# Performance work log

Measured on AMD Instinct MI355X. Metric: run time of the kernel, lower is better.

Reference implementation:

```python
import jax, jax.numpy as jnp
import numpy as np
import math

B, S, D, H, F = 2, 2048, 1024, 16, 4096
HD = D // H  # head size 64
EPS = 1e-5


def layernorm(x, g, b):
    mu = jnp.mean(x, axis=-1, keepdims=True)
    var = jnp.mean((x - mu) ** 2, axis=-1, keepdims=True)
    return (x - mu) * jax.lax.rsqrt(var + EPS) * g + b


def new_gelu(x):
    c = math.sqrt(2.0 / math.pi)
    return 0.5 * x * (1.0 + jnp.tanh(c * (x + 0.044715 * x ** 3)))


def setup_inputs() -> dict:
    key = jax.random.key(0)
    ks = jax.random.split(key, 20)
    sc = 0.02
    return {
        "x": jax.random.normal(ks[0], (B, S, D), jnp.float32),
        # per-head q/k/v weights stacked: [H, HD, D] (torch Linear weight layout [out,in])
        "Wq": jax.random.normal(ks[1], (H, HD, D), jnp.float32) * sc,
        "bq": jax.random.normal(ks[2], (H, HD), jnp.float32) * sc,
        "Wk": jax.random.normal(ks[3], (H, HD, D), jnp.float32) * sc,
        "bk": jax.random.normal(ks[4], (H, HD), jnp.float32) * sc,
        "Wv": jax.random.normal(ks[5], (H, HD, D), jnp.float32) * sc,
        "bv": jax.random.normal(ks[6], (H, HD), jnp.float32) * sc,
        "Wo": jax.random.normal(ks[7], (D, D), jnp.float32) * sc,
        "bo": jax.random.normal(ks[8], (D,), jnp.float32) * sc,
        "ln1_g": 1.0 + jax.random.normal(ks[9], (D,), jnp.float32) * sc,
        "ln1_b": jax.random.normal(ks[10], (D,), jnp.float32) * sc,
        "W1": jax.random.normal(ks[11], (F, D), jnp.float32) * sc,
        "b1": jax.random.normal(ks[12], (F,), jnp.float32) * sc,
        "W2": jax.random.normal(ks[13], (D, F), jnp.float32) * sc,
        "b2": jax.random.normal(ks[14], (D,), jnp.float32) * sc,
        "ln2_g": 1.0 + jax.random.normal(ks[15], (D,), jnp.float32) * sc,
        "ln2_b": jax.random.normal(ks[16], (D,), jnp.float32) * sc,
    }


def reference(x, Wq, bq, Wk, bk, Wv, bv, Wo, bo, ln1_g, ln1_b, W1, b1, W2, b2, ln2_g, ln2_b):
    # --- pre-LN multi-head attention (dropout is identity in eval) ---
    h = layernorm(x, ln1_g, ln1_b)
    q = jnp.einsum("bsd,hed->bshe", h, Wq) + bq  # [B,S,H,HD]
    k = jnp.einsum("bsd,hed->bshe", h, Wk) + bk
    v = jnp.einsum("bsd,hed->bshe", h, Wv) + bv
    scores = jnp.einsum("bshe,bthe->bhst", q, k) / math.sqrt(HD)
    probs = jax.nn.softmax(scores, axis=-1)
    attn = jnp.einsum("bhst,bthe->bshe", probs, v).reshape(B, S, D)  # concat heads
    attn = attn @ Wo.T + bo
    x = x + attn
    # --- pre-LN MLP with NewGELU ---
    h2 = layernorm(x, ln2_g, ln2_b)
    mlp = new_gelu(h2 @ W1.T + b1) @ W2.T + b2
    return x + mlp
```

## Files before the change

### kernel.cpp

```cpp
#include <hip/hip_runtime.h>

typedef unsigned short u16;
typedef __attribute__((ext_vector_type(8))) __bf16 bf16x8;
typedef __attribute__((ext_vector_type(4))) __bf16 bf16x4;
typedef __attribute__((ext_vector_type(4))) float f32x4;
typedef __attribute__((ext_vector_type(4))) unsigned short u16x4;

#define AS1 __attribute__((address_space(1)))
#define AS3 __attribute__((address_space(3)))

__device__ __forceinline__ void async_load16(const void* g, void* l) {
  __builtin_amdgcn_global_load_lds((const AS1 void*)g, (AS3 void*)l, 16, 0, 0);
}

__device__ __forceinline__ float exp2_fast(float x) {
#if __has_builtin(__builtin_amdgcn_exp2f)
  return __builtin_amdgcn_exp2f(x);
#else
  return exp2f(x);
#endif
}
__device__ __forceinline__ float rcp_fast(float x) {
#if __has_builtin(__builtin_amdgcn_rcpf)
  return __builtin_amdgcn_rcpf(x);
#else
  return 1.0f / x;
#endif
}

__device__ __forceinline__ u16 f2bf(float f) {
  union { float f; unsigned u; } a; a.f = f;
  unsigned u = a.u;
  u += 0x7fffu + ((u >> 16) & 1u);
  return (u16)(u >> 16);
}
__device__ __forceinline__ u16 bf_bits(float f) {
  union { __bf16 b; u16 u; } c; c.b = (__bf16)f; return c.u;
}

__global__ __launch_bounds__(256)
void f2b_kernel(const float* __restrict__ s, u16* __restrict__ d, int n4) {
  int i = blockIdx.x * 256 + threadIdx.x;
  if (i >= n4) return;
  const float4 v = ((const float4*)s)[i];
  u16x4 o; o[0] = f2bf(v.x); o[1] = f2bf(v.y); o[2] = f2bf(v.z); o[3] = f2bf(v.w);
  ((u16x4*)d)[i] = o;
}

__global__ __launch_bounds__(256)
void ln_kernel(const float* __restrict__ x, const float* __restrict__ g,
               const float* __restrict__ b, u16* __restrict__ out) {
  const int row = blockIdx.x, tid = threadIdx.x;
  const float4 v = ((const float4*)(x + (size_t)row * 1024))[tid];
  float s = v.x + v.y + v.z + v.w;
  float s2 = v.x * v.x + v.y * v.y + v.z * v.z + v.w * v.w;
#pragma unroll
  for (int o = 1; o < 64; o <<= 1) { s += __shfl_xor(s, o); s2 += __shfl_xor(s2, o); }
  __shared__ float red[8];
  const int wave = tid >> 6, lane = tid & 63;
  if (lane == 0) { red[wave] = s; red[wave + 4] = s2; }
  __syncthreads();
  s = red[0] + red[1] + red[2] + red[3];
  s2 = red[4] + red[5] + red[6] + red[7];
  const float mu = s * (1.f / 1024.f);
  const float rstd = rsqrtf(s2 * (1.f / 1024.f) - mu * mu + 1e-5f);
  const float4 gg = ((const float4*)g)[tid];
  const float4 bb = ((const float4*)b)[tid];
  u16x4 o4;
  o4[0] = f2bf((v.x - mu) * rstd * gg.x + bb.x);
  o4[1] = f2bf((v.y - mu) * rstd * gg.y + bb.y);
  o4[2] = f2bf((v.z - mu) * rstd * gg.z + bb.z);
  o4[3] = f2bf((v.w - mu) * rstd * gg.w + bb.w);
  ((u16x4*)(out + (size_t)row * 1024))[tid] = o4;
}

__global__ __launch_bounds__(256)
void ln_fuse(const float* __restrict__ x, const float* __restrict__ p0,
             const float* __restrict__ p1, const float* __restrict__ bo,
             const float* __restrict__ g, const float* __restrict__ b,
             float* __restrict__ out, u16* __restrict__ hb) {
  const int row = blockIdx.x, tid = threadIdx.x;
  const size_t base = (size_t)row * 1024;
  const float4 xv = ((const float4*)(x + base))[tid];
  const float4 a0 = ((const float4*)(p0 + base))[tid];
  const float4 a1 = ((const float4*)(p1 + base))[tid];
  const float4 bv = ((const float4*)bo)[tid];
  float4 t;
  t.x = xv.x + a0.x + a1.x + bv.x;
  t.y = xv.y + a0.y + a1.y + bv.y;
  t.z = xv.z + a0.z + a1.z + bv.z;
  t.w = xv.w + a0.w + a1.w + bv.w;
  ((float4*)(out + base))[tid] = t;
  float s = t.x + t.y + t.z + t.w;
  float s2 = t.x * t.x + t.y * t.y + t.z * t.z + t.w * t.w;
#pragma unroll
  for (int o = 1; o < 64; o <<= 1) { s += __shfl_xor(s, o); s2 += __shfl_xor(s2, o); }
  __shared__ float red[8];
  const int wave = tid >> 6, lane = tid & 63;
  if (lane == 0) { red[wave] = s; red[wave + 4] = s2; }
  __syncthreads();
  s = red[0] + red[1] + red[2] + red[3];
  s2 = red[4] + red[5] + red[6] + red[7];
  const float mu = s * (1.f / 1024.f);
  const float rstd = rsqrtf(s2 * (1.f / 1024.f) - mu * mu + 1e-5f);
  const float4 gg = ((const float4*)g)[tid];
  const float4 bb = ((const float4*)b)[tid];
  u16x4 o4;
  o4[0] = f2bf((t.x - mu) * rstd * gg.x + bb.x);
  o4[1] = f2bf((t.y - mu) * rstd * gg.y + bb.y);
  o4[2] = f2bf((t.z - mu) * rstd * gg.z + bb.z);
  o4[3] = f2bf((t.w - mu) * rstd * gg.w + bb.w);
  ((u16x4*)(hb + base))[tid] = o4;
}

__global__ __launch_bounds__(256)
void add2(float* __restrict__ out, const float* __restrict__ m0,
          const float* __restrict__ m1, const float* __restrict__ b2) {
  const int i = blockIdx.x * 256 + threadIdx.x;
  const float4 o = ((const float4*)out)[i];
  const float4 a = ((const float4*)m0)[i];
  const float4 c = ((const float4*)m1)[i];
  const float4 bv = ((const float4*)b2)[i & 255];
  float4 r;
  r.x = o.x + a.x + c.x + bv.x;
  r.y = o.y + a.y + c.y + bv.y;
  r.z = o.z + a.z + c.z + bv.z;
  r.w = o.w + a.w + c.w + bv.w;
  ((float4*)out)[i] = r;
}

template <class Epi>
__global__ __launch_bounds__(256)
void gemm_bt(const u16* __restrict__ A, const u16* __restrict__ Bw,
             int ldk, int K, Epi epi) {
  __shared__ __align__(16) u16 As[128 * 32];
  __shared__ __align__(16) u16 Bs[128 * 32];
  const int tid = threadIdx.x;
  const int wave = tid >> 6, lane = tid & 63;
  const int quad = lane >> 4, l16 = lane & 15;
  const int bm = blockIdx.x * 128, bn = blockIdx.y * 128;
  const int kz = blockIdx.z;
  const int wm = (wave & 1) * 64, wn = (wave >> 1) * 64;

  const int srow = lane >> 2, scol = (lane & 3) * 8;
  const u16* pa0 = A + (size_t)(bm + wave * 32 + srow) * ldk + (size_t)kz * K + scol;
  const u16* pa1 = pa0 + (size_t)16 * ldk;
  const u16* pb0 = Bw + (size_t)(bn + wave * 32 + srow) * ldk + (size_t)kz * K + scol;
  const u16* pb1 = pb0 + (size_t)16 * ldk;
  u16* la0 = &As[wave * 1024];
  u16* la1 = la0 + 512;
  u16* lb0 = &Bs[wave * 1024];
  u16* lb1 = lb0 + 512;

  const f32x4 fz = {0.f, 0.f, 0.f, 0.f};
  f32x4 acc[4][4];
#pragma unroll
  for (int i = 0; i < 4; i++)
#pragma unroll
    for (int j = 0; j < 4; j++) acc[i][j] = fz;

  for (int k0 = 0; k0 < K; k0 += 32) {
    async_load16(pa0, la0);
    async_load16(pa1, la1);
    async_load16(pb0, lb0);
    async_load16(pb1, lb1);
    pa0 += 32; pa1 += 32; pb0 += 32; pb1 += 32;
    __syncthreads();
    bf16x8 af[4], bfr[4];
#pragma unroll
    for (int mi = 0; mi < 4; mi++)
      af[mi] = *(const bf16x8*)&As[(wm + mi * 16 + l16) * 32 + quad * 8];
#pragma unroll
    for (int ni = 0; ni < 4; ni++)
      bfr[ni] = *(const bf16x8*)&Bs[(wn + ni * 16 + l16) * 32 + quad * 8];
#pragma unroll
    for (int mi = 0; mi < 4; mi++)
#pragma unroll
      for (int ni = 0; ni < 4; ni++)
        acc[mi][ni] = __builtin_amdgcn_mfma_f32_16x16x32_bf16(af[mi], bfr[ni], acc[mi][ni], 0, 0, 0);
    __syncthreads();
  }
#pragma unroll
  for (int mi = 0; mi < 4; mi++)
#pragma unroll
    for (int ni = 0; ni < 4; ni++)
      epi(bm + wm + mi * 16 + quad * 4, bn + wn + ni * 16 + l16, kz, acc[mi][ni]);
}

struct EpiQKV {
  u16 *q, *k, *vt; const float *bq, *bk, *bv;
  __device__ void operator()(int m0, int n, int, f32x4 v) const {
    const int which = n >> 10, nn = n & 1023;
    const int hh = nn >> 6, e = nn & 63;
    const int bb = m0 >> 11, s0 = m0 & 2047;
    const size_t bh = (size_t)(bb * 16 + hh);
    if (which == 0) {
      const float bias = bq[nn];
      u16* p = &q[(bh * 2048 + s0) * 64 + e];
#pragma unroll
      for (int r = 0; r < 4; r++) p[r * 64] = bf_bits((v[r] + bias) * 0.18033688f);
    } else if (which == 1) {
      const float bias = bk[nn];
      u16* p = &k[(bh * 2048 + s0) * 64 + e];
#pragma unroll
      for (int r = 0; r < 4; r++) p[r * 64] = bf_bits(v[r] + bias);
    } else {
      const float bias = bv[nn];
      bf16x4 pk;
#pragma unroll
      for (int r = 0; r < 4; r++) pk[r] = (__bf16)(v[r] + bias);
      *(bf16x4*)&vt[(bh * 64 + e) * 2048 + s0] = pk;
    }
  }
};
struct EpiPart {
  float *p0, *p1;
  __device__ void operator()(int m0, int n, int kz, f32x4 v) const {
    float* p = kz ? p1 : p0;
#pragma unroll
    for (int r = 0; r < 4; r++) p[(size_t)(m0 + r) * 1024 + n] = v[r];
  }
};
struct EpiGelu {
  const float* b1; u16* o;
  __device__ void operator()(int m0, int n, int, f32x4 v) const {
    const float bias = b1[n];
#pragma unroll
    for (int r = 0; r < 4; r++) {
      const float u = v[r] + bias;
      const float z2 = u * (2.3021183f + 0.10294515f * u * u);
      const float d = 1.0f + exp2_fast(-z2);
      o[(size_t)(m0 + r) * 4096 + n] = bf_bits(u * rcp_fast(d));
    }
  }
};

__global__ __launch_bounds__(256)
void attn_kernel(const u16* __restrict__ Q, const u16* __restrict__ K,
                 const u16* __restrict__ Vt, u16* __restrict__ O) {
  __shared__ __align__(16) u16 Ks[64 * 72];
  __shared__ __align__(16) u16 Vs[64 * 72];
  __shared__ __align__(16) u16 Ps[4][32 * 72];
  const int tid = threadIdx.x, wave = tid >> 6, lane = tid & 63;
  const int quad = lane >> 4, l16 = lane & 15;
  const int b = blockIdx.z, h = blockIdx.y, qt = blockIdx.x;
  const size_t bh = (size_t)(b * 16 + h);
  const u16* Qp = Q + bh * (size_t)(2048 * 64);
  const u16* Kp = K + bh * (size_t)(2048 * 64);
  const u16* Vp = Vt + bh * (size_t)(64 * 2048);
  const int q0 = qt * 128 + wave * 32;

  bf16x8 qf[2][2];
#pragma unroll
  for (int rg = 0; rg < 2; rg++) {
    const u16* qrow = &Qp[(size_t)(q0 + rg * 16 + l16) * 64 + quad * 8];
    qf[rg][0] = *(const bf16x8*)qrow;
    qf[rg][1] = *(const bf16x8*)(qrow + 32);
  }

  const int sr = tid >> 2, sc = (tid & 3) * 16;
  const int krow = 4 * (sr & 15) + (sr >> 4);
  const u16* kg = &Kp[(size_t)krow * 64 + sc];
  const u16* vg = &Vp[(size_t)sr * 2048 + sc];
  u16* kl = &Ks[sr * 72 + sc];
  u16* vl = &Vs[sr * 72 + sc];
  u16* Pw = &Ps[wave][0];

  bf16x8 ones;
#pragma unroll
  for (int i = 0; i < 8; i++) ones[i] = (__bf16)1.0f;

  const f32x4 fz = {0.f, 0.f, 0.f, 0.f};
  f32x4 acc[2][4], lsum[2];
#pragma unroll
  for (int rg = 0; rg < 2; rg++) {
    lsum[rg] = fz;
#pragma unroll
    for (int g = 0; g < 4; g++) acc[rg][g] = fz;
  }

  bf16x8 pk0 = *(const bf16x8*)kg, pk1 = *(const bf16x8*)(kg + 8);
  bf16x8 pv0 = *(const bf16x8*)vg, pv1 = *(const bf16x8*)(vg + 8);

  for (int t0 = 0; t0 < 2048; t0 += 64) {
    *(bf16x8*)kl = pk0; *(bf16x8*)(kl + 8) = pk1;
    *(bf16x8*)vl = pv0; *(bf16x8*)(vl + 8) = pv1;
    __syncthreads();
    kg += 64 * 64; vg += 64;
    pk0 = *(const bf16x8*)kg; pk1 = *(const bf16x8*)(kg + 8);
    pv0 = *(const bf16x8*)vg; pv1 = *(const bf16x8*)(vg + 8);

    f32x4 s[2][4];
#pragma unroll
    for (int g = 0; g < 4; g++) {
      const u16* kr = &Ks[(g * 16 + l16) * 72 + quad * 8];
      const bf16x8 kb0 = *(const bf16x8*)kr;
      const bf16x8 kb1 = *(const bf16x8*)(kr + 32);
#pragma unroll
      for (int rg = 0; rg < 2; rg++) {
        f32x4 z = __builtin_amdgcn_mfma_f32_16x16x32_bf16(qf[rg][0], kb0, fz, 0, 0, 0);
        s[rg][g] = __builtin_amdgcn_mfma_f32_16x16x32_bf16(qf[rg][1], kb1, z, 0, 0, 0);
      }
    }
#pragma unroll
    for (int rg = 0; rg < 2; rg++)
#pragma unroll
      for (int r = 0; r < 4; r++) {
        f32x4 pf;
#pragma unroll
        for (int g = 0; g < 4; g++) pf[g] = exp2_fast(s[rg][g][r]);
        const bf16x4 pb = __builtin_convertvector(pf, bf16x4);
        *(bf16x4*)&Pw[(rg * 16 + quad * 4 + r) * 72 + 4 * l16] = pb;
      }
    bf16x8 pa[2][2];
#pragma unroll
    for (int rg = 0; rg < 2; rg++) {
      const u16* pr = &Pw[(rg * 16 + l16) * 72 + quad * 8];
      pa[rg][0] = *(const bf16x8*)pr;
      pa[rg][1] = *(const bf16x8*)(pr + 32);
      lsum[rg] = __builtin_amdgcn_mfma_f32_16x16x32_bf16(pa[rg][0], ones, lsum[rg], 0, 0, 0);
      lsum[rg] = __builtin_amdgcn_mfma_f32_16x16x32_bf16(pa[rg][1], ones, lsum[rg], 0, 0, 0);
    }
#pragma unroll
    for (int g = 0; g < 4; g++) {
      const u16* vr = &Vs[(g * 16 + l16) * 72 + quad * 8];
      const bf16x8 vb0 = *(const bf16x8*)vr;
      const bf16x8 vb1 = *(const bf16x8*)(vr + 32);
#pragma unroll
      for (int rg = 0; rg < 2; rg++) {
        acc[rg][g] = __builtin_amdgcn_mfma_f32_16x16x32_bf16(pa[rg][0], vb0, acc[rg][g], 0, 0, 0);
        acc[rg][g] = __builtin_amdgcn_mfma_f32_16x16x32_bf16(pa[rg][1], vb1, acc[rg][g], 0, 0, 0);
      }
    }
    __syncthreads();
  }
#pragma unroll
  for (int rg = 0; rg < 2; rg++)
#pragma unroll
    for (int r = 0; r < 4; r++) {
      const float inv = rcp_fast(lsum[rg][r]);
      const int s_row = q0 + rg * 16 + quad * 4 + r;
      u16* op = (u16*)&O[((size_t)(b * 2048 + s_row)) * 1024 + h * 64 + l16];
#pragma unroll
      for (int g = 0; g < 4; g++) op[g * 16] = bf_bits(acc[rg][g][r] * inv);
    }
}

extern "C" void kernel_launch(void* const* d_in, const int* in_sizes, int n_in,
                              void* d_out, int out_size, void* d_ws, size_t ws_size,
                              hipStream_t stream) {
  const float* x   = (const float*)d_in[0];
  const float* Wq  = (const float*)d_in[1];
  const float* bq  = (const float*)d_in[2];
  const float* Wk  = (const float*)d_in[3];
  const float* bk  = (const float*)d_in[4];
  const float* Wv  = (const float*)d_in[5];
  const float* bv  = (const float*)d_in[6];
  const float* Wo  = (const float*)d_in[7];
  const float* bo  = (const float*)d_in[8];
  const float* g1  = (const float*)d_in[9];
  const float* be1 = (const float*)d_in[10];
  const float* W1  = (const float*)d_in[11];
  const float* b1  = (const float*)d_in[12];
  const float* W2  = (const float*)d_in[13];
  const float* b2  = (const float*)d_in[14];
  const float* g2  = (const float*)d_in[15];
  const float* be2 = (const float*)d_in[16];
  float* out = (float*)d_out;

  char* w = (char*)d_ws;
  u16* wqkv = (u16*)w; w += (size_t)3072 * 1024 * 2;
  u16* wob  = (u16*)w; w += (size_t)1024 * 1024 * 2;
  u16* w1b  = (u16*)w; w += (size_t)4096 * 1024 * 2;
  u16* w2b  = (u16*)w; w += (size_t)1024 * 4096 * 2;
  u16* hb   = (u16*)w; w += (size_t)4096 * 1024 * 2;
  u16* qb   = (u16*)w; w += (size_t)4096 * 1024 * 2;
  u16* kb   = (u16*)w; w += (size_t)4096 * 1024 * 2;
  u16* vtb  = (u16*)w; w += (size_t)4096 * 1024 * 2;
  u16* atb  = (u16*)w; w += (size_t)4096 * 1024 * 2;
  u16* m1b  = (u16*)w; w += (size_t)4096 * 4096 * 2;

  float* p0 = (float*)m1b;
  float* p1 = (float*)(m1b + 4096 * 2048);
  float* m0 = (float*)qb;
  float* m1 = (float*)vtb;

  f2b_kernel<<<1024, 256, 0, stream>>>(Wq, wqkv, 262144);
  f2b_kernel<<<1024, 256, 0, stream>>>(Wk, wqkv + 1024 * 1024, 262144);
  f2b_kernel<<<1024, 256, 0, stream>>>(Wv, wqkv + 2 * 1024 * 1024, 262144);
  f2b_kernel<<<1024, 256, 0, stream>>>(Wo, wob, 262144);
  f2b_kernel<<<4096, 256, 0, stream>>>(W1, w1b, 1048576);
  f2b_kernel<<<4096, 256, 0, stream>>>(W2, w2b, 1048576);

  ln_kernel<<<4096, 256, 0, stream>>>(x, g1, be1, hb);
  gemm_bt<EpiQKV><<<dim3(32, 24, 1), 256, 0, stream>>>(hb, wqkv, 1024, 1024,
      EpiQKV{qb, kb, vtb, bq, bk, bv});
  attn_kernel<<<dim3(16, 16, 2), 256, 0, stream>>>(qb, kb, vtb, atb);
  gemm_bt<EpiPart><<<dim3(32, 8, 2), 256, 0, stream>>>(atb, wob, 1024, 512,
      EpiPart{p0, p1});
  ln_fuse<<<4096, 256, 0, stream>>>(x, p0, p1, bo, g2, be2, out, hb);
  gemm_bt<EpiGelu><<<dim3(32, 32, 1), 256, 0, stream>>>(hb, w1b, 1024, 1024,
      EpiGelu{b1, m1b});
  gemm_bt<EpiPart><<<dim3(32, 8, 2), 256, 0, stream>>>(m1b, w2b, 4096, 2048,
      EpiPart{m0, m1});
  add2<<<4096, 256, 0, stream>>>(out, m0, m1, b2);
}
```

Baseline: 391.9 us.

## Store split-K partials as bf16, use 4-way split for W2, merge weight casts

```diff
diff --git a/kernel.cpp b/kernel.cpp
--- a/kernel.cpp
+++ b/kernel.cpp
@@ -37,14 +37,27 @@
 __device__ __forceinline__ u16 bf_bits(float f) {
   union { __bf16 b; u16 u; } c; c.b = (__bf16)f; return c.u;
 }
-
-__global__ __launch_bounds__(256)
-void f2b_kernel(const float* __restrict__ s, u16* __restrict__ d, int n4) {
-  int i = blockIdx.x * 256 + threadIdx.x;
-  if (i >= n4) return;
-  const float4 v = ((const float4*)s)[i];
+__device__ __forceinline__ float bf2f(u16 h) {
+  union { unsigned u; float f; } c; c.u = ((unsigned)h) << 16; return c.f;
+}
+
+__global__ __launch_bounds__(256)
+void f2b_all(const float* __restrict__ s0, const float* __restrict__ s1,
+             const float* __restrict__ s2, const float* __restrict__ s3,
+             const float* __restrict__ s4, const float* __restrict__ s5,
+             u16* __restrict__ dst) {
+  const int i = blockIdx.x * 256 + threadIdx.x;
+  const float* s; int off;
+  if (i < 1048576) {
+    if (i < 262144)      { s = s0; off = i; }
+    else if (i < 524288) { s = s1; off = i - 262144; }
+    else if (i < 786432) { s = s2; off = i - 524288; }
+    else                 { s = s3; off = i - 786432; }
+  } else if (i < 2097152) { s = s4; off = i - 1048576; }
+  else                    { s = s5; off = i - 2097152; }
+  const float4 v = ((const float4*)s)[off];
   u16x4 o; o[0] = f2bf(v.x); o[1] = f2bf(v.y); o[2] = f2bf(v.z); o[3] = f2bf(v.w);
-  ((u16x4*)d)[i] = o;
+  ((u16x4*)dst)[i] = o;
 }
 
 __global__ __launch_bounds__(256)
@@ -75,21 +88,22 @@
 }
 
 __global__ __launch_bounds__(256)
-void ln_fuse(const float* __restrict__ x, const float* __restrict__ p0,
-             const float* __restrict__ p1, const float* __restrict__ bo,
-             const float* __restrict__ g, const float* __restrict__ b,
-             float* __restrict__ out, u16* __restrict__ hb) {
+void ln_fuse(const float* __restrict__ x, const u16* __restrict__ parts,
+             const float* __restrict__ bo, const float* __restrict__ g,
+             const float* __restrict__ b, float* __restrict__ out,
+             u16* __restrict__ hb) {
   const int row = blockIdx.x, tid = threadIdx.x;
   const size_t base = (size_t)row * 1024;
+  const int i4 = row * 256 + tid;
   const float4 xv = ((const float4*)(x + base))[tid];
-  const float4 a0 = ((const float4*)(p0 + base))[tid];
-  const float4 a1 = ((const float4*)(p1 + base))[tid];
+  const u16x4 h0 = ((const u16x4*)parts)[i4];
+  const u16x4 h1 = ((const u16x4*)(parts + 4194304))[i4];
   const float4 bv = ((const float4*)bo)[tid];
   float4 t;
-  t.x = xv.x + a0.x + a1.x + bv.x;
-  t.y = xv.y + a0.y + a1.y + bv.y;
-  t.z = xv.z + a0.z + a1.z + bv.z;
-  t.w = xv.w + a0.w + a1.w + bv.w;
+  t.x = xv.x + bf2f(h0[0]) + bf2f(h1[0]) + bv.x;
+  t.y = xv.y + bf2f(h0[1]) + bf2f(h1[1]) + bv.y;
+  t.z = xv.z + bf2f(h0[2]) + bf2f(h1[2]) + bv.z;
+  t.w = xv.w + bf2f(h0[3]) + bf2f(h1[3]) + bv.w;
   ((float4*)(out + base))[tid] = t;
   float s = t.x + t.y + t.z + t.w;
   float s2 = t.x * t.x + t.y * t.y + t.z * t.z + t.w * t.w;
@@ -114,18 +128,18 @@
 }
 
 __global__ __launch_bounds__(256)
-void add2(float* __restrict__ out, const float* __restrict__ m0,
-          const float* __restrict__ m1, const float* __restrict__ b2) {
+void add4(float* __restrict__ out, const u16* __restrict__ p,
+          const float* __restrict__ b2) {
   const int i = blockIdx.x * 256 + threadIdx.x;
   const float4 o = ((const float4*)out)[i];
-  const float4 a = ((const float4*)m0)[i];
-  const float4 c = ((const float4*)m1)[i];
   const float4 bv = ((const float4*)b2)[i & 255];
-  float4 r;
-  r.x = o.x + a.x + c.x + bv.x;
-  r.y = o.y + a.y + c.y + bv.y;
-  r.z = o.z + a.z + c.z + bv.z;
-  r.w = o.w + a.w + c.w + bv.w;
+  float a0 = o.x + bv.x, a1 = o.y + bv.y, a2 = o.z + bv.z, a3 = o.w + bv.w;
+#pragma unroll
+  for (int kz = 0; kz < 4; kz++) {
+    const u16x4 h = ((const u16x4*)(p + (size_t)kz * 4194304))[i];
+    a0 += bf2f(h[0]); a1 += bf2f(h[1]); a2 += bf2f(h[2]); a3 += bf2f(h[3]);
+  }
+  float4 r; r.x = a0; r.y = a1; r.z = a2; r.w = a3;
   ((float4*)out)[i] = r;
 }
 
@@ -213,12 +227,12 @@
     }
   }
 };
-struct EpiPart {
-  float *p0, *p1;
+struct EpiPartB {
+  u16* p;
   __device__ void operator()(int m0, int n, int kz, f32x4 v) const {
-    float* p = kz ? p1 : p0;
-#pragma unroll
-    for (int r = 0; r < 4; r++) p[(size_t)(m0 + r) * 1024 + n] = v[r];
+    u16* pp = p + (size_t)kz * 4194304;
+#pragma unroll
+    for (int r = 0; r < 4; r++) pp[(size_t)(m0 + r) * 1024 + n] = bf_bits(v[r]);
   }
 };
 struct EpiGelu {
@@ -380,28 +394,21 @@
   u16* atb  = (u16*)w; w += (size_t)4096 * 1024 * 2;
   u16* m1b  = (u16*)w; w += (size_t)4096 * 4096 * 2;
 
-  float* p0 = (float*)m1b;
-  float* p1 = (float*)(m1b + 4096 * 2048);
-  float* m0 = (float*)qb;
-  float* m1 = (float*)vtb;
-
-  f2b_kernel<<<1024, 256, 0, stream>>>(Wq, wqkv, 262144);
-  f2b_kernel<<<1024, 256, 0, stream>>>(Wk, wqkv + 1024 * 1024, 262144);
-  f2b_kernel<<<1024, 256, 0, stream>>>(Wv, wqkv + 2 * 1024 * 1024, 262144);
-  f2b_kernel<<<1024, 256, 0, stream>>>(Wo, wob, 262144);
-  f2b_kernel<<<4096, 256, 0, stream>>>(W1, w1b, 1048576);
-  f2b_kernel<<<4096, 256, 0, stream>>>(W2, w2b, 1048576);
+  u16* op_part = m1b;
+  u16* ml_part = qb;
+
+  f2b_all<<<12288, 256, 0, stream>>>(Wq, Wk, Wv, Wo, W1, W2, wqkv);
 
   ln_kernel<<<4096, 256, 0, stream>>>(x, g1, be1, hb);
   gemm_bt<EpiQKV><<<dim3(32, 24, 1), 256, 0, stream>>>(hb, wqkv, 1024, 1024,
       EpiQKV{qb, kb, vtb, bq, bk, bv});
   attn_kernel<<<dim3(16, 16, 2), 256, 0, stream>>>(qb, kb, vtb, atb);
-  gemm_bt<EpiPart><<<dim3(32, 8, 2), 256, 0, stream>>>(atb, wob, 1024, 512,
-      EpiPart{p0, p1});
-  ln_fuse<<<4096, 256, 0, stream>>>(x, p0, p1, bo, g2, be2, out, hb);
+  gemm_bt<EpiPartB><<<dim3(32, 8, 2), 256, 0, stream>>>(atb, wob, 1024, 512,
+      EpiPartB{op_part});
+  ln_fuse<<<4096, 256, 0, stream>>>(x, op_part, bo, g2, be2, out, hb);
   gemm_bt<EpiGelu><<<dim3(32, 32, 1), 256, 0, stream>>>(hb, w1b, 1024, 1024,
       EpiGelu{b1, m1b});
-  gemm_bt<EpiPart><<<dim3(32, 8, 2), 256, 0, stream>>>(m1b, w2b, 4096, 2048,
-      EpiPart{m0, m1});
-  add2<<<4096, 256, 0, stream>>>(out, m0, m1, b2);
-}
+  gemm_bt<EpiPartB><<<dim3(32, 8, 4), 256, 0, stream>>>(m1b, w2b, 4096, 1024,
+      EpiPartB{ml_part});
+  add4<<<4096, 256, 0, stream>>>(out, ml_part, b2);
+}
```

Result: no change. 385.6 us (-1.6%).
